# Optimization experiments

Measured on AMD Instinct MI355X. Metric: run time of the kernel, lower is better.

Reference implementation:

```python
import jax, jax.numpy as jnp
import numpy as np

FEATURES_DIM = 64 * (64 * 10 + 1)  # 41024
BASE = 64 * 10 + 1                 # 641
B = 1024


def encode_boards(boards):
    """Vectorized HalfKP encode. boards: [B,8,8] int in 0..12.
    0 = my king, 12 = opp king, 6 = empty, 1..5 my pieces, 7..11 opp pieces.
    Returns [B, 2*FEATURES_DIM] float32 = concat(opps, mys) per original code."""
    nb = boards.shape[0]
    d = boards.reshape(nb, 64)
    sq = jnp.arange(64, dtype=jnp.int32)
    my_king = jnp.argmax(d == 0, axis=1).astype(jnp.int32)    # [B]
    opp_king = jnp.argmax(d == 12, axis=1).astype(jnp.int32)  # [B]
    is_my = (d >= 1) & (d <= 5)
    is_opp = (d >= 7) & (d <= 11)
    # MY_PIECE_TYPES index = piece-1 ; OPP_PIECE_TYPES [11,10,9,8,7] index = 11-piece
    my_idx = my_king[:, None] * BASE + (d - 1) * 64 + sq
    opp_idx = opp_king[:, None] * BASE + (11 - d) * 64 + sq
    my_idx = jnp.where(is_my, my_idx, FEATURES_DIM)    # out-of-range -> dropped
    opp_idx = jnp.where(is_opp, opp_idx, FEATURES_DIM)
    rows = jnp.arange(nb)[:, None]
    mys = jnp.zeros((nb, FEATURES_DIM), jnp.float32).at[rows, my_idx].set(1.0, mode='drop')
    opps = jnp.zeros((nb, FEATURES_DIM), jnp.float32).at[rows, opp_idx].set(1.0, mode='drop')
    return jnp.concatenate([opps, mys], axis=1)


def setup_inputs() -> dict:
    key = jax.random.key(0)
    ks = jax.random.split(key, 12)
    # boards: values 1..11 everywhere, then place exactly one my-king (0) and one opp-king (12)
    bf = jax.random.randint(ks[0], (B, 64), 1, 12, dtype=jnp.int32)
    mk = jax.random.randint(ks[1], (B,), 0, 32)
    ok = jax.random.randint(ks[2], (B,), 32, 64)
    rows = jnp.arange(B)
    bf = bf.at[rows, mk].set(0).at[rows, ok].set(12)
    boards = bf.reshape(B, 8, 8)
    s = 0.02
    W_my = jax.random.normal(ks[3], (256, FEATURES_DIM), jnp.float32) * s
    b_my = jax.random.normal(ks[4], (256,), jnp.float32) * s
    W_opp = jax.random.normal(ks[5], (256, FEATURES_DIM), jnp.float32) * s
    b_opp = jax.random.normal(ks[6], (256,), jnp.float32) * s
    W1 = jax.random.normal(ks[7], (32, 512), jnp.float32) * s
    b1 = jnp.zeros((32,), jnp.float32)
    W2 = jax.random.normal(ks[8], (32, 32), jnp.float32) * s
    b2 = jnp.zeros((32,), jnp.float32)
    W3 = jax.random.normal(ks[9], (1, 32), jnp.float32) * s
    b3 = jnp.zeros((1,), jnp.float32)
    return {"boards": boards, "W_my": W_my, "b_my": b_my, "W_opp": W_opp,
            "b_opp": b_opp, "W1": W1, "b1": b1, "W2": W2, "b2": b2,
            "W3": W3, "b3": b3}


def reference(boards, W_my, b_my, W_opp, b_opp, W1, b1, W2, b2, W3, b3):
    feats = encode_boards(boards)              # [B, 2*FEATURES_DIM] = (opps, mys)
    # NOTE: faithful to original: my_pieces consumes the FIRST half (which is opps)
    my_in = feats[:, :FEATURES_DIM]
    opp_in = feats[:, FEATURES_DIM:]
    my_pos = jax.nn.relu(my_in @ W_my.T + b_my)     # [B,256]
    opp_pos = jax.nn.relu(opp_in @ W_opp.T + b_opp) # [B,256]
    h = jnp.concatenate([my_pos, opp_pos], axis=1)  # [B,512]
    h = jax.nn.relu(h @ W1.T + b1)
    h = jax.nn.relu(h @ W2.T + b2)
    out = h @ W3.T + b3                             # [B,1]
    return out.reshape(-1)
```

## Files before the change

kernel.cpp:

```cpp
#include <hip/hip_runtime.h>

#define FD    41024
#define KBASE 641
#define WIN   320
#define NROW  256

__global__ __launch_bounds__(320) void transpose_windows(
    const float* __restrict__ W_my, const float* __restrict__ W_opp,
    float* __restrict__ Wt)
{
    __shared__ float tile[32][WIN + 1];
    const int blk = blockIdx.x;
    const int rq  = blk & 3;
    const int k   = (blk >> 2) & 63;
    const int m   = blk >> 8;
    const float* __restrict__ W = m ? W_opp : W_my;
    const int t = threadIdx.x;
    const size_t colbase = (size_t)k * KBASE;
    float* __restrict__ dst = Wt + (((size_t)m * 64 + k) * WIN) * NROW;

    for (int chunk = 0; chunk < 2; chunk++) {
        const int rbase = rq * 64 + chunk * 32;
        for (int rr = 0; rr < 32; rr++)
            tile[rr][t] = W[(size_t)(rbase + rr) * FD + colbase + t];
        __syncthreads();
        const int rsub  = t & 31;
        const int cbase = t >> 5;
        for (int it = 0; it < 32; it++) {
            const int c = cbase + it * 10;
            dst[(size_t)c * NROW + rbase + rsub] = tile[rsub][c];
        }
        __syncthreads();
    }
}

__global__ __launch_bounds__(256) void nnue_fwd_t(
    const int*   __restrict__ boards, const float* __restrict__ Wt,
    const float* __restrict__ b_my,  const float* __restrict__ b_opp,
    const float* __restrict__ W1,    const float* __restrict__ b1,
    const float* __restrict__ W2,    const float* __restrict__ b2,
    const float* __restrict__ W3,    const float* __restrict__ b3,
    float* __restrict__ out)
{
    __shared__ int   s_off0[64];
    __shared__ int   s_off1[64];
    __shared__ int   s_cnt[2];
    __shared__ int   s_kings[2];
    __shared__ float s_red0[4][256];
    __shared__ float s_red1[4][256];
    __shared__ float s_h[512];
    __shared__ float s_h1[32];

    const int b = blockIdx.x;
    const int t = threadIdx.x;

    if (t < 2) s_cnt[t] = 0;
    __syncthreads();

    if (t < 64) {
        int d = boards[b * 64 + t];
        if (d == 0)       s_kings[0] = t;
        else if (d == 12) s_kings[1] = t;
        else if (d >= 1 && d <= 5) { int p = atomicAdd(&s_cnt[1], 1); s_off1[p] = (d - 1) * 64 + t; }
        else if (d >= 7)           { int p = atomicAdd(&s_cnt[0], 1); s_off0[p] = (11 - d) * 64 + t; }
    }
    __syncthreads();

    const int n0 = s_cnt[0], n1 = s_cnt[1];
    const int g  = t >> 6;
    const int r4 = (t & 63) << 2;
    const float* __restrict__ w0 = Wt + (size_t)s_kings[1] * (WIN * NROW);
    const float* __restrict__ w1 = Wt + ((size_t)64 + (size_t)s_kings[0]) * (WIN * NROW);

    float4 a0 = make_float4(0.f, 0.f, 0.f, 0.f);
    float4 a1 = make_float4(0.f, 0.f, 0.f, 0.f);
    for (int i = g; i < n0; i += 4) {
        const float4 v = *(const float4*)(w0 + s_off0[i] * NROW + r4);
        a0.x += v.x; a0.y += v.y; a0.z += v.z; a0.w += v.w;
    }
    for (int i = g; i < n1; i += 4) {
        const float4 v = *(const float4*)(w1 + s_off1[i] * NROW + r4);
        a1.x += v.x; a1.y += v.y; a1.z += v.z; a1.w += v.w;
    }
    ((float4*)s_red0[g])[t & 63] = a0;
    ((float4*)s_red1[g])[t & 63] = a1;
    __syncthreads();

    {
        float h0 = b_my[t]  + ((s_red0[0][t] + s_red0[1][t]) + (s_red0[2][t] + s_red0[3][t]));
        float h1 = b_opp[t] + ((s_red1[0][t] + s_red1[1][t]) + (s_red1[2][t] + s_red1[3][t]));
        s_h[t]       = fmaxf(h0, 0.0f);
        s_h[256 + t] = fmaxf(h1, 0.0f);
    }
    __syncthreads();

    {
        const int o = t >> 3, l = t & 7;
        const float* __restrict__ w = W1 + o * 512;
        float p = 0.0f;
        for (int k = l; k < 512; k += 8) p += s_h[k] * w[k];
        p += __shfl_down(p, 4, 8);
        p += __shfl_down(p, 2, 8);
        p += __shfl_down(p, 1, 8);
        if (l == 0) s_h1[o] = fmaxf(p + b1[o], 0.0f);
    }
    __syncthreads();

    if (t < 32) {
        const float* __restrict__ w = W2 + t * 32;
        float acc = b2[t];
        for (int k = 0; k < 32; k++) acc += s_h1[k] * w[k];
        float h2 = fmaxf(acc, 0.0f);
        float p = h2 * W3[t];
        p += __shfl_down(p, 16, 32);
        p += __shfl_down(p,  8, 32);
        p += __shfl_down(p,  4, 32);
        p += __shfl_down(p,  2, 32);
        p += __shfl_down(p,  1, 32);
        if (t == 0) out[b] = p + b3[0];
    }
}

__global__ __launch_bounds__(256) void nnue_fwd(
    const int*   __restrict__ boards,
    const float* __restrict__ W_my,  const float* __restrict__ b_my,
    const float* __restrict__ W_opp, const float* __restrict__ b_opp,
    const float* __restrict__ W1,    const float* __restrict__ b1,
    const float* __restrict__ W2,    const float* __restrict__ b2,
    const float* __restrict__ W3,    const float* __restrict__ b3,
    float* __restrict__ out)
{
    __shared__ int   s_off0[64];
    __shared__ int   s_off1[64];
    __shared__ int   s_cnt[2];
    __shared__ int   s_kings[2];
    __shared__ float s_h[512];
    __shared__ float s_h1[32];

    const int b = blockIdx.x;
    const int t = threadIdx.x;

    if (t < 2) s_cnt[t] = 0;
    __syncthreads();

    if (t < 64) {
        int d = boards[b * 64 + t];
        if (d == 0)       s_kings[0] = t;
        else if (d == 12) s_kings[1] = t;
        else if (d >= 1 && d <= 5) { int p = atomicAdd(&s_cnt[1], 1); s_off1[p] = (d - 1) * 64 + t; }
        else if (d >= 7)           { int p = atomicAdd(&s_cnt[0], 1); s_off0[p] = (11 - d) * 64 + t; }
    }
    __syncthreads();

    const int n0 = s_cnt[0], n1 = s_cnt[1];
    const int base0 = s_kings[1] * KBASE;
    const int base1 = s_kings[0] * KBASE;

    {
        const float* __restrict__ w = W_my + (size_t)t * FD + base0;
        float acc = b_my[t];
        for (int i = 0; i < n0; i++) acc += w[s_off0[i]];
        s_h[t] = fmaxf(acc, 0.0f);
    }
    {
        const float* __restrict__ w = W_opp + (size_t)t * FD + base1;
        float acc = b_opp[t];
        for (int i = 0; i < n1; i++) acc += w[s_off1[i]];
        s_h[256 + t] = fmaxf(acc, 0.0f);
    }
    __syncthreads();

    {
        const int o = t >> 3, l = t & 7;
        const float* __restrict__ w = W1 + o * 512;
        float p = 0.0f;
        for (int k = l; k < 512; k += 8) p += s_h[k] * w[k];
        p += __shfl_down(p, 4, 8);
        p += __shfl_down(p, 2, 8);
        p += __shfl_down(p, 1, 8);
        if (l == 0) s_h1[o] = fmaxf(p + b1[o], 0.0f);
    }
    __syncthreads();

    if (t < 32) {
        const float* __restrict__ w = W2 + t * 32;
        float acc = b2[t];
        for (int k = 0; k < 32; k++) acc += s_h1[k] * w[k];
        float h2 = fmaxf(acc, 0.0f);
        float p = h2 * W3[t];
        p += __shfl_down(p, 16, 32);
        p += __shfl_down(p,  8, 32);
        p += __shfl_down(p,  4, 32);
        p += __shfl_down(p,  2, 32);
        p += __shfl_down(p,  1, 32);
        if (t == 0) out[b] = p + b3[0];
    }
}

extern "C" void kernel_launch(void* const* d_in, const int* in_sizes, int n_in,
                              void* d_out, int out_size, void* d_ws, size_t ws_size,
                              hipStream_t stream) {
    const int*   boards = (const int*)  d_in[0];
    const float* W_my   = (const float*)d_in[1];
    const float* b_my   = (const float*)d_in[2];
    const float* W_opp  = (const float*)d_in[3];
    const float* b_opp  = (const float*)d_in[4];
    const float* W1     = (const float*)d_in[5];
    const float* b1     = (const float*)d_in[6];
    const float* W2     = (const float*)d_in[7];
    const float* b2     = (const float*)d_in[8];
    const float* W3     = (const float*)d_in[9];
    const float* b3     = (const float*)d_in[10];
    float* out = (float*)d_out;

    const int nb = in_sizes[0] / 64;
    const size_t wt_bytes = (size_t)2 * 64 * WIN * NROW * sizeof(float);

    if (ws_size >= wt_bytes) {
        float* Wt = (float*)d_ws;
        transpose_windows<<<512, 320, 0, stream>>>(W_my, W_opp, Wt);
        nnue_fwd_t<<<nb, 256, 0, stream>>>(boards, Wt, b_my, b_opp,
                                           W1, b1, W2, b2, W3, b3, out);
    } else {
        nnue_fwd<<<nb, 256, 0, stream>>>(boards, W_my, b_my, W_opp, b_opp,
                                         W1, b1, W2, b2, W3, b3, out);
    }
}
```

Baseline: 147.2 us.

## Bucket boards by king square and gather from shared-memory weight windows

Replaces the full weight-window transpose plus per-board gather with a three-kernel pipeline. A classify kernel writes per-board feature offsets and king squares to workspace. A bucketed gather kernel then loads each (king, 32-row) weight window into LDS once and accumulates all boards sharing that king. A separate MLP tail finishes the network. This avoids writing and re-reading a transposed copy of the weight windows, at the cost of an extra launch, a pass over all boards per block to build its bucket list, and only moderate parallelism when buckets are small.

```diff
diff --git a/kernel.cpp b/kernel.cpp
--- a/kernel.cpp
+++ b/kernel.cpp
@@ -3,102 +3,136 @@
 #define FD    41024
 #define KBASE 641
 #define WIN   320
-#define NROW  256
-
-__global__ __launch_bounds__(320) void transpose_windows(
+#define NB_MAX 1024
+
+#define WS_OFF0  0
+#define WS_OFF1  (NB_MAX*64)
+#define WS_N0    (2*NB_MAX*64)
+#define WS_N1    (WS_N0 + NB_MAX)
+#define WS_KMY   (WS_N1 + NB_MAX)
+#define WS_KOPP  (WS_KMY + NB_MAX)
+#define WS_H     (WS_KOPP + NB_MAX)
+
+__global__ __launch_bounds__(64) void classify(
+    const int* __restrict__ boards, int* __restrict__ ws)
+{
+    __shared__ int s_off0[64], s_off1[64];
+    __shared__ int s_cnt[2], s_k[2];
+    const int b = blockIdx.x;
+    const int t = threadIdx.x;
+
+    s_off0[t] = 0; s_off1[t] = 0;
+    if (t < 2) s_cnt[t] = 0;
+    __syncthreads();
+
+    const int d = boards[b * 64 + t];
+    if (d == 0)       s_k[0] = t;
+    else if (d == 12) s_k[1] = t;
+    else if (d >= 1 && d <= 5) { int p = atomicAdd(&s_cnt[1], 1); s_off1[p] = (d - 1) * 64 + t; }
+    else if (d >= 7 && d <= 11){ int p = atomicAdd(&s_cnt[0], 1); s_off0[p] = (11 - d) * 64 + t; }
+    __syncthreads();
+
+    ws[WS_OFF0 + b * 64 + t] = s_off0[t];
+    ws[WS_OFF1 + b * 64 + t] = s_off1[t];
+    if (t == 0) {
+        ws[WS_N0   + b] = s_cnt[0];
+        ws[WS_N1   + b] = s_cnt[1];
+        ws[WS_KMY  + b] = s_k[0];
+        ws[WS_KOPP + b] = s_k[1];
+    }
+}
+
+__global__ __launch_bounds__(256) void gather_bucketed(
     const float* __restrict__ W_my, const float* __restrict__ W_opp,
-    float* __restrict__ Wt)
-{
-    __shared__ float tile[32][WIN + 1];
+    const int* __restrict__ ws, float* __restrict__ h, int nb)
+{
+    __shared__ float win[WIN * 33];
+    __shared__ int   list[NB_MAX];
+    __shared__ int   goffs[8 * 64];
+    __shared__ int   lcnt;
+
     const int blk = blockIdx.x;
-    const int rq  = blk & 3;
-    const int k   = (blk >> 2) & 63;
-    const int m   = blk >> 8;
+    const int rg  = blk & 7;
+    const int k   = (blk >> 3) & 63;
+    const int m   = blk >> 9;
+    const int t   = threadIdx.x;
+
+    if (t == 0) lcnt = 0;
+    __syncthreads();
+
+    const int* __restrict__ karr = ws + (m ? WS_KMY : WS_KOPP);
+    for (int i = t; i < nb; i += 256)
+        if (karr[i] == k) { int p = atomicAdd(&lcnt, 1); list[p] = i; }
+    __syncthreads();
+
+    const int n_b = lcnt;
+    if (n_b == 0) return;
+
     const float* __restrict__ W = m ? W_opp : W_my;
-    const int t = threadIdx.x;
-    const size_t colbase = (size_t)k * KBASE;
-    float* __restrict__ dst = Wt + (((size_t)m * 64 + k) * WIN) * NROW;
-
-    for (int chunk = 0; chunk < 2; chunk++) {
-        const int rbase = rq * 64 + chunk * 32;
-        for (int rr = 0; rr < 32; rr++)
-            tile[rr][t] = W[(size_t)(rbase + rr) * FD + colbase + t];
-        __syncthreads();
-        const int rsub  = t & 31;
-        const int cbase = t >> 5;
-        for (int it = 0; it < 32; it++) {
-            const int c = cbase + it * 10;
-            dst[(size_t)c * NROW + rbase + rsub] = tile[rsub][c];
+    const size_t gbase = (size_t)(rg * 32) * FD + (size_t)k * KBASE;
+    for (int idx = t; idx < 32 * WIN; idx += 256) {
+        const int r = idx / WIN;
+        const int c = idx - r * WIN;
+        win[c * 33 + r] = W[gbase + (size_t)r * FD + c];
+    }
+    __syncthreads();
+
+    const int* __restrict__ offarr = ws + (m ? WS_OFF1 : WS_OFF0);
+    const int* __restrict__ narr   = ws + (m ? WS_N1   : WS_N0);
+    const int r    = t & 31;
+    const int slot = t >> 5;
+    const int hcol = m * 256 + rg * 32 + r;
+
+    for (int g = 0; g < n_b; g += 8) {
+        for (int j = t; j < 8 * 64; j += 256) {
+            const int bi = g + (j >> 6);
+            if (bi < n_b) goffs[j] = offarr[list[bi] * 64 + (j & 63)];
         }
         __syncthreads();
-    }
-}
-
-__global__ __launch_bounds__(256) void nnue_fwd_t(
-    const int*   __restrict__ boards, const float* __restrict__ Wt,
+
+        const int bi = g + slot;
+        if (bi < n_b) {
+            const int board = list[bi];
+            const int nf = narr[board];
+            const int* __restrict__ lo = &goffs[slot * 64];
+            float acc = 0.0f;
+            int i = 0;
+            for (; i + 4 <= nf; i += 4) {
+                float a0 = win[lo[i]     * 33 + r];
+                float a1 = win[lo[i + 1] * 33 + r];
+                float a2 = win[lo[i + 2] * 33 + r];
+                float a3 = win[lo[i + 3] * 33 + r];
+                acc += ((a0 + a1) + (a2 + a3));
+            }
+            for (; i < nf; i++) acc += win[lo[i] * 33 + r];
+            h[(size_t)board * 512 + hcol] = acc;
+        }
+        __syncthreads();
+    }
+}
+
+__global__ __launch_bounds__(256) void mlp_tail(
+    const float* __restrict__ h,
     const float* __restrict__ b_my,  const float* __restrict__ b_opp,
     const float* __restrict__ W1,    const float* __restrict__ b1,
     const float* __restrict__ W2,    const float* __restrict__ b2,
     const float* __restrict__ W3,    const float* __restrict__ b3,
     float* __restrict__ out)
 {
-    __shared__ int   s_off0[64];
-    __shared__ int   s_off1[64];
-    __shared__ int   s_cnt[2];
-    __shared__ int   s_kings[2];
-    __shared__ float s_red0[4][256];
-    __shared__ float s_red1[4][256];
     __shared__ float s_h[512];
     __shared__ float s_h1[32];
-
     const int b = blockIdx.x;
     const int t = threadIdx.x;
 
-    if (t < 2) s_cnt[t] = 0;
-    __syncthreads();
-
-    if (t < 64) {
-        int d = boards[b * 64 + t];
-        if (d == 0)       s_kings[0] = t;
-        else if (d == 12) s_kings[1] = t;
-        else if (d >= 1 && d <= 5) { int p = atomicAdd(&s_cnt[1], 1); s_off1[p] = (d - 1) * 64 + t; }
-        else if (d >= 7)           { int p = atomicAdd(&s_cnt[0], 1); s_off0[p] = (11 - d) * 64 + t; }
-    }
-    __syncthreads();
-
-    const int n0 = s_cnt[0], n1 = s_cnt[1];
-    const int g  = t >> 6;
-    const int r4 = (t & 63) << 2;
-    const float* __restrict__ w0 = Wt + (size_t)s_kings[1] * (WIN * NROW);
-    const float* __restrict__ w1 = Wt + ((size_t)64 + (size_t)s_kings[0]) * (WIN * NROW);
-
-    float4 a0 = make_float4(0.f, 0.f, 0.f, 0.f);
-    float4 a1 = make_float4(0.f, 0.f, 0.f, 0.f);
-    for (int i = g; i < n0; i += 4) {
-        const float4 v = *(const float4*)(w0 + s_off0[i] * NROW + r4);
-        a0.x += v.x; a0.y += v.y; a0.z += v.z; a0.w += v.w;
-    }
-    for (int i = g; i < n1; i += 4) {
-        const float4 v = *(const float4*)(w1 + s_off1[i] * NROW + r4);
-        a1.x += v.x; a1.y += v.y; a1.z += v.z; a1.w += v.w;
-    }
-    ((float4*)s_red0[g])[t & 63] = a0;
-    ((float4*)s_red1[g])[t & 63] = a1;
-    __syncthreads();
-
-    {
-        float h0 = b_my[t]  + ((s_red0[0][t] + s_red0[1][t]) + (s_red0[2][t] + s_red0[3][t]));
-        float h1 = b_opp[t] + ((s_red1[0][t] + s_red1[1][t]) + (s_red1[2][t] + s_red1[3][t]));
-        s_h[t]       = fmaxf(h0, 0.0f);
-        s_h[256 + t] = fmaxf(h1, 0.0f);
-    }
+    s_h[t]       = fmaxf(h[(size_t)b * 512 + t]       + b_my[t],  0.0f);
+    s_h[256 + t] = fmaxf(h[(size_t)b * 512 + 256 + t] + b_opp[t], 0.0f);
     __syncthreads();
 
     {
         const int o = t >> 3, l = t & 7;
         const float* __restrict__ w = W1 + o * 512;
         float p = 0.0f;
-        for (int k = l; k < 512; k += 8) p += s_h[k] * w[k];
+        for (int kk = l; kk < 512; kk += 8) p += s_h[kk] * w[kk];
         p += __shfl_down(p, 4, 8);
         p += __shfl_down(p, 2, 8);
         p += __shfl_down(p, 1, 8);
@@ -109,7 +143,7 @@
     if (t < 32) {
         const float* __restrict__ w = W2 + t * 32;
         float acc = b2[t];
-        for (int k = 0; k < 32; k++) acc += s_h1[k] * w[k];
+        for (int kk = 0; kk < 32; kk++) acc += s_h1[kk] * w[kk];
         float h2 = fmaxf(acc, 0.0f);
         float p = h2 * W3[t];
         p += __shfl_down(p, 16, 32);
@@ -174,7 +208,7 @@
         const int o = t >> 3, l = t & 7;
         const float* __restrict__ w = W1 + o * 512;
         float p = 0.0f;
-        for (int k = l; k < 512; k += 8) p += s_h[k] * w[k];
+        for (int kk = l; kk < 512; kk += 8) p += s_h[kk] * w[kk];
         p += __shfl_down(p, 4, 8);
         p += __shfl_down(p, 2, 8);
         p += __shfl_down(p, 1, 8);
@@ -185,7 +219,7 @@
     if (t < 32) {
         const float* __restrict__ w = W2 + t * 32;
         float acc = b2[t];
-        for (int k = 0; k < 32; k++) acc += s_h1[k] * w[k];
+        for (int kk = 0; kk < 32; kk++) acc += s_h1[kk] * w[kk];
         float h2 = fmaxf(acc, 0.0f);
         float p = h2 * W3[t];
         p += __shfl_down(p, 16, 32);
@@ -214,13 +248,14 @@
     float* out = (float*)d_out;
 
     const int nb = in_sizes[0] / 64;
-    const size_t wt_bytes = (size_t)2 * 64 * WIN * NROW * sizeof(float);
-
-    if (ws_size >= wt_bytes) {
-        float* Wt = (float*)d_ws;
-        transpose_windows<<<512, 320, 0, stream>>>(W_my, W_opp, Wt);
-        nnue_fwd_t<<<nb, 256, 0, stream>>>(boards, Wt, b_my, b_opp,
-                                           W1, b1, W2, b2, W3, b3, out);
+    const size_t ws_needed = (size_t)(WS_H + (size_t)NB_MAX * 512) * sizeof(int);
+
+    if (nb <= NB_MAX && ws_size >= ws_needed) {
+        int*   wsi = (int*)d_ws;
+        float* h   = (float*)d_ws + WS_H;
+        classify<<<nb, 64, 0, stream>>>(boards, wsi);
+        gather_bucketed<<<1024, 256, 0, stream>>>(W_my, W_opp, wsi, h, nb);
+        mlp_tail<<<nb, 256, 0, stream>>>(h, b_my, b_opp, W1, b1, W2, b2, W3, b3, out);
     } else {
         nnue_fwd<<<nb, 256, 0, stream>>>(boards, W_my, b_my, W_opp, b_opp,
                                          W1, b1, W2, b2, W3, b3, out);
```

Measured after the change: 148.6 us. No clear change (+0.9%).
